# Kernel optimization log

Hardware: AMD Instinct MI355X
Metric: run time of the kernel (lower is better)

## Reference

```python
import jax, jax.numpy as jnp
import numpy as np

N_HEADS, D_MODEL, D_HEAD = 12, 768, 64
INIT_RANGE = 0.02
IGNORE = -100000.0

def setup_inputs() -> dict:
    key = jax.random.key(0)
    ks = jax.random.split(key, 5)
    x = jax.random.normal(ks[0], (4, 2048, D_MODEL), dtype=jnp.float32)
    W_Q = jax.random.normal(ks[1], (N_HEADS, D_MODEL, D_HEAD), dtype=jnp.float32) * INIT_RANGE
    W_K = jax.random.normal(ks[2], (N_HEADS, D_MODEL, D_HEAD), dtype=jnp.float32) * INIT_RANGE
    W_V = jax.random.normal(ks[3], (N_HEADS, D_MODEL, D_HEAD), dtype=jnp.float32) * INIT_RANGE
    W_O = jax.random.normal(ks[4], (N_HEADS, D_HEAD, D_MODEL), dtype=jnp.float32) * INIT_RANGE
    b_Q = jnp.zeros((N_HEADS, D_HEAD), dtype=jnp.float32)
    b_K = jnp.zeros((N_HEADS, D_HEAD), dtype=jnp.float32)
    b_V = jnp.zeros((N_HEADS, D_HEAD), dtype=jnp.float32)
    b_O = jnp.zeros((D_MODEL,), dtype=jnp.float32)
    return {"normalized_resid_pre": x, "W_Q": W_Q, "b_Q": b_Q, "W_K": W_K,
            "b_K": b_K, "W_V": W_V, "b_V": b_V, "W_O": W_O, "b_O": b_O}

def reference(normalized_resid_pre, W_Q, b_Q, W_K, b_K, W_V, b_V, W_O, b_O):
    x = normalized_resid_pre  # [b, s, d_model]
    q = jnp.einsum('bsd,hde->bshe', x, W_Q) + b_Q  # [b, s, h, d_head]
    k = jnp.einsum('bsd,hde->bshe', x, W_K) + b_K
    v = jnp.einsum('bsd,hde->bshe', x, W_V) + b_V
    scores = jnp.einsum('bqhe,bkhe->bhqk', q, k) / jnp.sqrt(jnp.float32(D_HEAD))
    S = x.shape[1]
    causal = jnp.triu(jnp.ones((S, S), dtype=bool), k=1)  # True above diagonal
    scores = jnp.where(causal, jnp.float32(IGNORE), scores)
    pattern = jax.nn.softmax(scores, axis=-1)  # [b, h, q, k]
    z = jnp.einsum('bhqk,bkhe->bqhe', pattern, v)
    attn_out = jnp.einsum('bqhe,hed->bqd', z, W_O) + b_O
    return attn_out
```

## Files before the change

kernel.cpp:

```cpp
#include <hip/hip_runtime.h>

typedef unsigned short u16;
typedef __bf16 bf16x8 __attribute__((ext_vector_type(8)));
typedef float f32x4 __attribute__((ext_vector_type(4)));

#define D_MODEL 768
#define NH 12
#define SEQ 2048
#define BB 4
#define QSCALE 0.18033688011112042f
#define FIXM 8.0f

__device__ __forceinline__ u16 f2b(float f) {
  __bf16 h = (__bf16)f;
  return __builtin_bit_cast(u16, h);
}

__device__ __forceinline__ void gload16(const void* g, void* l) {
  __builtin_amdgcn_global_load_lds((__attribute__((address_space(1))) void*)g,
                                   (__attribute__((address_space(3))) void*)l, 16, 0, 0);
}

__device__ __forceinline__ f32x4 mm16(bf16x8 a, bf16x8 b, f32x4 c) {
  return __builtin_amdgcn_mfma_f32_16x16x32_bf16(a, b, c, 0, 0, 0);
}

__global__ void prep_kernel(const float* __restrict__ x, const float* __restrict__ wq,
                            const float* __restrict__ wk, const float* __restrict__ wv,
                            const float* __restrict__ wo, const float* __restrict__ bq,
                            const float* __restrict__ bk, const float* __restrict__ bv,
                            u16* __restrict__ xb, u16* __restrict__ wt,
                            u16* __restrict__ wot, float* __restrict__ qkvb) {
  const int bid = blockIdx.x;
  if (bid < 6144) {
    int i = (bid * 256 + threadIdx.x) * 4;
    float4 v = *(const float4*)&x[i];
    ushort4 o;
    o.x = f2b(v.x); o.y = f2b(v.y); o.z = f2b(v.z); o.w = f2b(v.w);
    *(ushort4*)&xb[i] = o;
  } else {
    int i = (bid - 6144) * 256 + threadIdx.x;
    {
      int cp = i / 768, d = i % 768;
      int proj = cp / 768, c = cp % 768, h = c / 64, e = c % 64;
      const float* W = (proj == 0) ? wq : ((proj == 1) ? wk : wv);
      float v = W[(size_t)h * 49152 + d * 64 + e];
      if (proj == 0) v *= QSCALE;
      wt[i] = f2b(v);
    }
    if (i < 768 * 768) {
      int rp = i / 768, d = i % 768;
      wot[i] = f2b(wo[(size_t)d * 768 + rp]);
    }
    if (i < 2304) {
      int proj = i / 768, c = i % 768;
      float v = (proj == 0) ? bq[c] * QSCALE : ((proj == 1) ? bk[c] : bv[c]);
      qkvb[i] = v;
    }
  }
}

__global__ __launch_bounds__(512) void gemm_qkv_kernel(
    const u16* __restrict__ A, const u16* __restrict__ Bt,
    const float* __restrict__ qkvb, u16* __restrict__ qw, u16* __restrict__ kw,
    u16* __restrict__ vw) {
  __shared__ u16 lds[73728];
  const int tid = threadIdx.x;
  const int w = tid >> 6, lane = tid & 63;
  const int lg = lane >> 4, cl = lane & 15;
  const int L = blockIdx.x;
  const int v = (L & 7) * 72 + (L >> 3);
  const int bm = v % 9, bn = v / 9;
  const int wr = w >> 1, wc = w & 1;
  const int NT = 12;

  f32x4 vzero = {0.f, 0.f, 0.f, 0.f};
  f32x4 acc[4][4];
#pragma unroll
  for (int mi = 0; mi < 4; mi++)
#pragma unroll
    for (int ni = 0; ni < 4; ni++) acc[mi][ni] = vzero;

  const u16* aB = A + (size_t)bm * 256 * D_MODEL;
  const u16* bB = Bt + (size_t)bn * 128 * D_MODEL;
  const int l8 = lane >> 3, l7 = lane & 7;

  auto stage = [&](int buf, int kt, int half) {
    const int kof = kt * 64;
#pragma unroll
    for (int j2 = 0; j2 < 2; j2++) {
      const int r0 = (w * 4 + half * 2 + j2) * 8;
      gload16(aB + (size_t)(r0 + l8) * D_MODEL + kof + l7 * 8,
              &lds[buf * 16384 + r0 * 64]);
    }
    const int r0b = (w * 2 + half) * 8;
    gload16(bB + (size_t)(r0b + l8) * D_MODEL + kof + l7 * 8,
            &lds[49152 + buf * 8192 + r0b * 64]);
  };

  stage(0, 0, 0); stage(0, 0, 1);
  stage(1, 1, 0); stage(1, 1, 1);
  asm volatile("s_waitcnt vmcnt(6)" ::: "memory");
  __builtin_amdgcn_s_barrier();

  for (int kt = 0; kt < NT; ++kt) {
    const int cA = (kt % 3) * 16384;
    const int cB = 49152 + (kt % 3) * 8192;
    const int nbuf = (kt + 2) % 3;
#pragma unroll
    for (int ks = 0; ks < 2; ks++) {
      bf16x8 af[4], bf4[4];
#pragma unroll
      for (int mi = 0; mi < 4; mi++)
        af[mi] = *(const bf16x8*)&lds[cA + (wr * 64 + mi * 16 + cl) * 64 + ks * 32 + lg * 8];
#pragma unroll
      for (int ni = 0; ni < 4; ni++)
        bf4[ni] = *(const bf16x8*)&lds[cB + (wc * 64 + ni * 16 + cl) * 64 + ks * 32 + lg * 8];
      if (kt + 2 < NT) stage(nbuf, kt + 2, ks);
      if (ks == 1) {
        if (kt + 2 < NT) asm volatile("s_waitcnt vmcnt(6)" ::: "memory");
        else asm volatile("s_waitcnt vmcnt(0)" ::: "memory");
      }
      __builtin_amdgcn_s_barrier();
      __builtin_amdgcn_s_setprio(1);
#pragma unroll
      for (int mi = 0; mi < 4; mi++)
#pragma unroll
        for (int ni = 0; ni < 4; ni++)
          acc[mi][ni] = mm16(af[mi], bf4[ni], acc[mi][ni]);
      __builtin_amdgcn_s_setprio(0);
      __builtin_amdgcn_s_barrier();
    }
  }

  __syncthreads();
  u16* lw = &lds[w * 4096];
  const int cm = bm * 256 + wr * 64;
  const int cn = bn * 128 + wc * 64;
  const int proj = cm / 768;
  const int h = (cm % 768) >> 6;
  const int b = cn >> 11, s_base = cn & 2047;
  const int rlo = lane >> 3, q8 = lane & 7;

  float bz[4][4];
#pragma unroll
  for (int mi = 0; mi < 4; mi++) {
    float4 b4 = *(const float4*)&qkvb[cm + mi * 16 + lg * 4];
    bz[mi][0] = b4.x; bz[mi][1] = b4.y; bz[mi][2] = b4.z; bz[mi][3] = b4.w;
  }

  if (proj < 2) {
#pragma unroll
    for (int mi = 0; mi < 4; mi++) {
      const int e0 = mi * 16 + lg * 4;
#pragma unroll
      for (int ni = 0; ni < 4; ni++) {
        const int s_l = ni * 16 + cl;
        ushort4 pk;
        pk.x = f2b(acc[mi][ni][0] + bz[mi][0]);
        pk.y = f2b(acc[mi][ni][1] + bz[mi][1]);
        pk.z = f2b(acc[mi][ni][2] + bz[mi][2]);
        pk.w = f2b(acc[mi][ni][3] + bz[mi][3]);
        *(ushort4*)&lw[(s_l * 128 + ((e0 * 2) ^ ((s_l & 7) << 4))) >> 1] = pk;
      }
    }
    u16* dst = ((proj == 0) ? qw : kw) + (((size_t)(b * NH + h) * SEQ + s_base) << 6);
#pragma unroll
    for (int it = 0; it < 8; it++) {
      const int row = it * 8 + rlo;
      *(bf16x8*)&dst[row * 64 + q8 * 8] =
          *(const bf16x8*)&lw[(row * 128 + ((q8 * 16) ^ ((row & 7) << 4))) >> 1];
    }
  } else {
#pragma unroll
    for (int mi = 0; mi < 4; mi++)
#pragma unroll
      for (int ni = 0; ni < 4; ni++) {
        const int s_l = ni * 16 + cl;
#pragma unroll
        for (int r = 0; r < 4; r++) {
          const int e_l = mi * 16 + lg * 4 + r;
          lw[(e_l * 128 + ((s_l * 2) ^ ((e_l & 7) << 4))) >> 1] =
              f2b(acc[mi][ni][r] + bz[mi][r]);
        }
      }
    u16* dst = vw + (((size_t)(b * NH + h)) << 17) + s_base;
#pragma unroll
    for (int it = 0; it < 8; it++) {
      const int row = it * 8 + rlo;
      *(bf16x8*)&dst[((size_t)row << 11) + q8 * 8] =
          *(const bf16x8*)&lw[(row * 128 + ((q8 * 16) ^ ((row & 7) << 4))) >> 1];
    }
  }
}

__global__ __launch_bounds__(512) void gemm_out_kernel(
    const u16* __restrict__ A, const u16* __restrict__ Bt,
    const float* __restrict__ bias0, float* __restrict__ outf) {
  __shared__ u16 lds[73728];
  const int tid = threadIdx.x;
  const int w = tid >> 6, lane = tid & 63;
  const int lg = lane >> 4, cl = lane & 15;
  const int L = blockIdx.x;
  const int v = (L & 7) * 24 + (L >> 3);
  const int bm = v / 6, bn = v % 6;
  const int wr = w >> 1, wc = w & 1;
  const int NT = 12;

  f32x4 vzero = {0.f, 0.f, 0.f, 0.f};
  f32x4 acc[4][4];
#pragma unroll
  for (int mi = 0; mi < 4; mi++)
#pragma unroll
    for (int ni = 0; ni < 4; ni++) acc[mi][ni] = vzero;

  const u16* aB = A + (size_t)bm * 256 * D_MODEL;
  const u16* bB = Bt + (size_t)bn * 128 * D_MODEL;
  const int l8 = lane >> 3, l7 = lane & 7;

  auto stage = [&](int buf, int kt, int half) {
    const int kof = kt * 64;
#pragma unroll
    for (int j2 = 0; j2 < 2; j2++) {
      const int r0 = (w * 4 + half * 2 + j2) * 8;
      gload16(aB + (size_t)(r0 + l8) * D_MODEL + kof + l7 * 8,
              &lds[buf * 16384 + r0 * 64]);
    }
    const int r0b = (w * 2 + half) * 8;
    gload16(bB + (size_t)(r0b + l8) * D_MODEL + kof + l7 * 8,
            &lds[49152 + buf * 8192 + r0b * 64]);
  };

  stage(0, 0, 0); stage(0, 0, 1);
  stage(1, 1, 0); stage(1, 1, 1);
  asm volatile("s_waitcnt vmcnt(6)" ::: "memory");
  __builtin_amdgcn_s_barrier();

  for (int kt = 0; kt < NT; ++kt) {
    const int cA = (kt % 3) * 16384;
    const int cB = 49152 + (kt % 3) * 8192;
    const int nbuf = (kt + 2) % 3;
#pragma unroll
    for (int ks = 0; ks < 2; ks++) {
      bf16x8 af[4], bf4[4];
#pragma unroll
      for (int mi = 0; mi < 4; mi++)
        af[mi] = *(const bf16x8*)&lds[cA + (wr * 64 + mi * 16 + cl) * 64 + ks * 32 + lg * 8];
#pragma unroll
      for (int ni = 0; ni < 4; ni++)
        bf4[ni] = *(const bf16x8*)&lds[cB + (wc * 64 + ni * 16 + cl) * 64 + ks * 32 + lg * 8];
      if (kt + 2 < NT) stage(nbuf, kt + 2, ks);
      if (ks == 1) {
        if (kt + 2 < NT) asm volatile("s_waitcnt vmcnt(6)" ::: "memory");
        else asm volatile("s_waitcnt vmcnt(0)" ::: "memory");
      }
      __builtin_amdgcn_s_barrier();
      __builtin_amdgcn_s_setprio(1);
#pragma unroll
      for (int mi = 0; mi < 4; mi++)
#pragma unroll
        for (int ni = 0; ni < 4; ni++)
          acc[mi][ni] = mm16(af[mi], bf4[ni], acc[mi][ni]);
      __builtin_amdgcn_s_setprio(0);
      __builtin_amdgcn_s_barrier();
    }
  }

  __syncthreads();
  u16* lw = &lds[w * 4096];
  float* lwf = (float*)lw;
  const int m_base = bm * 256 + wr * 64;
  const int n0 = bn * 128 + wc * 64;
  const int rlo = lane >> 3, q8 = lane & 7;
#pragma unroll
  for (int hh = 0; hh < 2; hh++) {
#pragma unroll
    for (int nn = 0; nn < 2; nn++) {
      const int ni = hh * 2 + nn;
      const float bz = bias0[n0 + ni * 16 + cl];
      const int col = nn * 16 + cl;
#pragma unroll
      for (int mi = 0; mi < 4; mi++)
#pragma unroll
        for (int r = 0; r < 4; r++) {
          const int row = mi * 16 + lg * 4 + r;
          lwf[(row * 128 + ((col * 4) ^ ((row & 7) << 4))) >> 2] = acc[mi][ni][r] + bz;
        }
    }
#pragma unroll
    for (int it = 0; it < 8; it++) {
      const int row = it * 8 + rlo;
      const int byt = row * 128 + ((q8 * 16) ^ ((row & 7) << 4));
      *(float4*)&outf[(size_t)(m_base + row) * D_MODEL + n0 + hh * 32 + q8 * 4] =
          *(const float4*)((const char*)lwf + byt);
    }
  }
}

__global__ __launch_bounds__(256) void attn_kernel(
    const u16* __restrict__ q_ws, const u16* __restrict__ k_ws,
    const u16* __restrict__ vT_ws, u16* __restrict__ z_ws) {
  __shared__ u16 lk[2][4096];
  __shared__ u16 lv[2][4096];
  __shared__ u16 lp[4096];
  const int tid = threadIdx.x, w = tid >> 6, lane = tid & 63;
  const int lg = lane >> 4, cl = lane & 15, c7 = cl & 7;
  const int L = blockIdx.x;
  const int vv = (L & 7) * 96 + (L >> 3);
  const int pair = vv & 15, bh = vv >> 4;
  const u16* qp = q_ws + (size_t)bh * SEQ * 64;
  const u16* kp = k_ws + (size_t)bh * SEQ * 64;
  const u16* vp = vT_ws + (size_t)bh * 64 * SEQ;
  const int b = bh / NH, h = bh % NH;

  const __bf16 one1 = (__bf16)1.0f;
  const bf16x8 vones = {one1, one1, one1, one1, one1, one1, one1, one1};

  for (int sel = 0; sel < 2; ++sel) {
    const int qt = (sel == 0) ? pair : 31 - pair;
    const int q0 = qt * 64;
    const int qabs = q0 + w * 16 + cl;

    bf16x8 qf[2];
#pragma unroll
    for (int ks = 0; ks < 2; ks++)
      qf[ks] = *(const bf16x8*)&qp[(size_t)(q0 + w * 16 + cl) * 64 + ks * 32 + lg * 8];

    f32x4 vzero = {0.f, 0.f, 0.f, 0.f};
    f32x4 accO[4];
#pragma unroll
    for (int nb = 0; nb < 4; nb++) accO[nb] = vzero;
    f32x4 accS = vzero;

#pragma unroll
    for (int c2 = 0; c2 < 2; c2++) {
      const int ch = w + c2 * 4;
      gload16(kp + (size_t)(lane)*64 + ch * 8, &lk[0][ch * 64 * 8]);
      gload16(vp + (size_t)lane * SEQ + ch * 8, &lv[0][ch * 64 * 8]);
    }
    asm volatile("s_waitcnt vmcnt(0)" ::: "memory");
    __builtin_amdgcn_s_barrier();

    for (int kt = 0; kt <= qt; ++kt) {
      const int cur = kt & 1;
      const int k0 = kt * 64;
      if (kt < qt) {
        const int kn = k0 + 64;
#pragma unroll
        for (int c2 = 0; c2 < 2; c2++) {
          const int ch = w + c2 * 4;
          gload16(kp + (size_t)(kn + lane) * 64 + ch * 8, &lk[cur ^ 1][ch * 64 * 8]);
          gload16(vp + (size_t)lane * SEQ + kn + ch * 8, &lv[cur ^ 1][ch * 64 * 8]);
        }
      }

      f32x4 sa[4];
#pragma unroll
      for (int cb = 0; cb < 4; cb++) sa[cb] = vzero;
      __builtin_amdgcn_s_setprio(1);
#pragma unroll
      for (int ks = 0; ks < 2; ks++) {
#pragma unroll
        for (int cb = 0; cb < 4; cb++) {
          bf16x8 kf = *(const bf16x8*)&lk[cur][((ks * 4 + lg) * 64 + cb * 16 + cl) * 8];
          sa[cb] = mm16(kf, qf[ks], sa[cb]);
        }
      }
      __builtin_amdgcn_s_setprio(0);
      if (kt == qt) {
#pragma unroll
        for (int cb = 0; cb < 4; cb++)
#pragma unroll
          for (int r = 0; r < 4; r++)
            if (k0 + cb * 16 + lg * 4 + r > qabs) sa[cb][r] = -1e30f;
      }

#pragma unroll
      for (int cb = 0; cb < 4; cb++) {
        float p0 = __builtin_amdgcn_exp2f(sa[cb][0] - FIXM);
        float p1 = __builtin_amdgcn_exp2f(sa[cb][1] - FIXM);
        float p2 = __builtin_amdgcn_exp2f(sa[cb][2] - FIXM);
        float p3 = __builtin_amdgcn_exp2f(sa[cb][3] - FIXM);
        ushort4 pk;
        pk.x = f2b(p0); pk.y = f2b(p1); pk.z = f2b(p2); pk.w = f2b(p3);
        *(ushort4*)&lp[w * 1024 + (cl * 128 + ((cb * 32 + lg * 8) ^ (c7 << 4))) / 2] = pk;
      }

      __builtin_amdgcn_s_setprio(1);
#pragma unroll
      for (int ks = 0; ks < 2; ks++) {
        bf16x8 pf = *(const bf16x8*)&lp[w * 1024 +
                                        (cl * 128 + ((ks * 64 + lg * 16) ^ (c7 << 4))) / 2];
#pragma unroll
        for (int nb = 0; nb < 4; nb++) {
          bf16x8 vf = *(const bf16x8*)&lv[cur][((ks * 4 + lg) * 64 + nb * 16 + cl) * 8];
          accO[nb] = mm16(pf, vf, accO[nb]);
        }
        accS = mm16(pf, vones, accS);
      }
      __builtin_amdgcn_s_setprio(0);

      asm volatile("s_waitcnt vmcnt(0)" ::: "memory");
      __builtin_amdgcn_s_barrier();
    }

    float inv[4];
#pragma unroll
    for (int r = 0; r < 4; r++) inv[r] = 1.f / accS[r];
#pragma unroll
    for (int nb = 0; nb < 4; nb++)
#pragma unroll
      for (int r = 0; r < 4; r++) {
        const int qrow = q0 + w * 16 + lg * 4 + r;
        z_ws[((size_t)b * SEQ + qrow) * D_MODEL + h * 64 + nb * 16 + cl] =
            f2b(accO[nb][r] * inv[r]);
      }
  }
}

extern "C" void kernel_launch(void* const* d_in, const int* in_sizes, int n_in,
                              void* d_out, int out_size, void* d_ws, size_t ws_size,
                              hipStream_t stream) {
  const float* x = (const float*)d_in[0];
  const float* wq = (const float*)d_in[1];
  const float* bq = (const float*)d_in[2];
  const float* wk = (const float*)d_in[3];
  const float* bk = (const float*)d_in[4];
  const float* wv = (const float*)d_in[5];
  const float* bv = (const float*)d_in[6];
  const float* wo = (const float*)d_in[7];
  const float* bo = (const float*)d_in[8];
  float* out = (float*)d_out;

  char* ws = (char*)d_ws;
  size_t off = 0;
  auto carve = [&](size_t bytes) -> u16* {
    u16* p = (u16*)(ws + off);
    off += (bytes + 255) & ~(size_t)255;
    return p;
  };
  u16* xb = carve((size_t)8192 * 768 * 2);
  u16* wt = carve((size_t)2304 * 768 * 2);
  u16* wot = carve((size_t)768 * 768 * 2);
  float* qkvb = (float*)carve((size_t)2304 * 4);
  u16* qw = carve((size_t)BB * NH * SEQ * 64 * 2);
  u16* kw = carve((size_t)BB * NH * SEQ * 64 * 2);
  u16* vw = carve((size_t)BB * NH * SEQ * 64 * 2);
  u16* zw = carve((size_t)8192 * 768 * 2);
  if (ws_size < off) return;

  prep_kernel<<<dim3(13056), dim3(256), 0, stream>>>(x, wq, wk, wv, wo, bq, bk, bv,
                                                     xb, wt, wot, qkvb);
  gemm_qkv_kernel<<<dim3(576), dim3(512), 0, stream>>>(wt, xb, qkvb, qw, kw, vw);
  attn_kernel<<<dim3(768), dim3(256), 0, stream>>>(qw, kw, vw, zw);
  gemm_out_kernel<<<dim3(192), dim3(512), 0, stream>>>(zw, wot, bo, out);
}
```

Measured before the change: 151.0 us.

## Give each attention block one query tile and feed P to MFMA from registers

The attention kernel now launches one block per (batch-head, query tile) instead of pairing a short and a long causal tile in one block. The grid doubles, and blocks are ordered longest tile first within each XCD to balance load. When the 16x16x16 bf16 MFMA builtin exists, the exp'd probabilities feed the PV product straight from registers, which removes the LDS round trip through lp and frees that shared memory. The cost is twice as many MFMA instructions with half the K depth, plus a longest-first ordering that relies on the hardware dispatching blocks in order.

```diff
diff --git a/kernel.cpp b/kernel.cpp
--- a/kernel.cpp
+++ b/kernel.cpp
@@ -2,6 +2,7 @@
 
 typedef unsigned short u16;
 typedef __bf16 bf16x8 __attribute__((ext_vector_type(8)));
+typedef short s16x4 __attribute__((ext_vector_type(4)));
 typedef float f32x4 __attribute__((ext_vector_type(4)));
 
 #define D_MODEL 768
@@ -11,6 +12,12 @@
 #define QSCALE 0.18033688011112042f
 #define FIXM 8.0f
 
+#if __has_builtin(__builtin_amdgcn_mfma_f32_16x16x16bf16_1k)
+#define HAVE_MM16 1
+#else
+#define HAVE_MM16 0
+#endif
+
 __device__ __forceinline__ u16 f2b(float f) {
   __bf16 h = (__bf16)f;
   return __builtin_bit_cast(u16, h);
@@ -24,6 +31,12 @@
 __device__ __forceinline__ f32x4 mm16(bf16x8 a, bf16x8 b, f32x4 c) {
   return __builtin_amdgcn_mfma_f32_16x16x32_bf16(a, b, c, 0, 0, 0);
 }
+
+#if HAVE_MM16
+__device__ __forceinline__ f32x4 mm16k(s16x4 a, s16x4 b, f32x4 c) {
+  return __builtin_amdgcn_mfma_f32_16x16x16bf16_1k(a, b, c, 0, 0, 0);
+}
+#endif
 
 __global__ void prep_kernel(const float* __restrict__ x, const float* __restrict__ wq,
                             const float* __restrict__ wk, const float* __restrict__ wv,
@@ -302,120 +315,146 @@
     const u16* __restrict__ vT_ws, u16* __restrict__ z_ws) {
   __shared__ u16 lk[2][4096];
   __shared__ u16 lv[2][4096];
+#if !HAVE_MM16
   __shared__ u16 lp[4096];
+#endif
   const int tid = threadIdx.x, w = tid >> 6, lane = tid & 63;
   const int lg = lane >> 4, cl = lane & 15, c7 = cl & 7;
   const int L = blockIdx.x;
-  const int vv = (L & 7) * 96 + (L >> 3);
-  const int pair = vv & 15, bh = vv >> 4;
+  const int xcd = L & 7, i = L >> 3;
+  const int qt = 31 - (i / 6);
+  const int bh = xcd * 6 + (i % 6);
   const u16* qp = q_ws + (size_t)bh * SEQ * 64;
   const u16* kp = k_ws + (size_t)bh * SEQ * 64;
   const u16* vp = vT_ws + (size_t)bh * 64 * SEQ;
   const int b = bh / NH, h = bh % NH;
 
+  const int q0 = qt * 64;
+  const int qabs = q0 + w * 16 + cl;
+
+  bf16x8 qf[2];
+#pragma unroll
+  for (int ks = 0; ks < 2; ks++)
+    qf[ks] = *(const bf16x8*)&qp[(size_t)(q0 + w * 16 + cl) * 64 + ks * 32 + lg * 8];
+
+  f32x4 vzero = {0.f, 0.f, 0.f, 0.f};
+  f32x4 accO[4];
+#pragma unroll
+  for (int nb = 0; nb < 4; nb++) accO[nb] = vzero;
+  f32x4 accS = vzero;
+
+#if HAVE_MM16
+  const short one_bf = (short)0x3F80;
+  const s16x4 ones4 = {one_bf, one_bf, one_bf, one_bf};
+#else
   const __bf16 one1 = (__bf16)1.0f;
   const bf16x8 vones = {one1, one1, one1, one1, one1, one1, one1, one1};
-
-  for (int sel = 0; sel < 2; ++sel) {
-    const int qt = (sel == 0) ? pair : 31 - pair;
-    const int q0 = qt * 64;
-    const int qabs = q0 + w * 16 + cl;
-
-    bf16x8 qf[2];
-#pragma unroll
-    for (int ks = 0; ks < 2; ks++)
-      qf[ks] = *(const bf16x8*)&qp[(size_t)(q0 + w * 16 + cl) * 64 + ks * 32 + lg * 8];
-
-    f32x4 vzero = {0.f, 0.f, 0.f, 0.f};
-    f32x4 accO[4];
-#pragma unroll
-    for (int nb = 0; nb < 4; nb++) accO[nb] = vzero;
-    f32x4 accS = vzero;
-
-#pragma unroll
-    for (int c2 = 0; c2 < 2; c2++) {
-      const int ch = w + c2 * 4;
-      gload16(kp + (size_t)(lane)*64 + ch * 8, &lk[0][ch * 64 * 8]);
-      gload16(vp + (size_t)lane * SEQ + ch * 8, &lv[0][ch * 64 * 8]);
-    }
+#endif
+
+#pragma unroll
+  for (int c2 = 0; c2 < 2; c2++) {
+    const int ch = w + c2 * 4;
+    gload16(kp + (size_t)(lane)*64 + ch * 8, &lk[0][ch * 64 * 8]);
+    gload16(vp + (size_t)lane * SEQ + ch * 8, &lv[0][ch * 64 * 8]);
+  }
+  asm volatile("s_waitcnt vmcnt(0)" ::: "memory");
+  __builtin_amdgcn_s_barrier();
+
+  for (int kt = 0; kt <= qt; ++kt) {
+    const int cur = kt & 1;
+    const int k0 = kt * 64;
+    if (kt < qt) {
+      const int kn = k0 + 64;
+#pragma unroll
+      for (int c2 = 0; c2 < 2; c2++) {
+        const int ch = w + c2 * 4;
+        gload16(kp + (size_t)(kn + lane) * 64 + ch * 8, &lk[cur ^ 1][ch * 64 * 8]);
+        gload16(vp + (size_t)lane * SEQ + kn + ch * 8, &lv[cur ^ 1][ch * 64 * 8]);
+      }
+    }
+
+    f32x4 sa[4];
+#pragma unroll
+    for (int cb = 0; cb < 4; cb++) sa[cb] = vzero;
+    __builtin_amdgcn_s_setprio(1);
+#pragma unroll
+    for (int ks = 0; ks < 2; ks++) {
+#pragma unroll
+      for (int cb = 0; cb < 4; cb++) {
+        bf16x8 kf = *(const bf16x8*)&lk[cur][((ks * 4 + lg) * 64 + cb * 16 + cl) * 8];
+        sa[cb] = mm16(kf, qf[ks], sa[cb]);
+      }
+    }
+    __builtin_amdgcn_s_setprio(0);
+    if (kt == qt) {
+#pragma unroll
+      for (int cb = 0; cb < 4; cb++)
+#pragma unroll
+        for (int r = 0; r < 4; r++)
+          if (k0 + cb * 16 + lg * 4 + r > qabs) sa[cb][r] = -1e30f;
+    }
+
+#if HAVE_MM16
+    s16x4 pa[4];
+#pragma unroll
+    for (int cb = 0; cb < 4; cb++) {
+#pragma unroll
+      for (int j = 0; j < 4; j++)
+        pa[cb][j] = (short)f2b(__builtin_amdgcn_exp2f(sa[cb][j] - FIXM));
+    }
+    __builtin_amdgcn_s_setprio(1);
+#pragma unroll
+    for (int cb = 0; cb < 4; cb++) {
+      accS = mm16k(pa[cb], ones4, accS);
+#pragma unroll
+      for (int nb = 0; nb < 4; nb++) {
+        const s16x4 vb = *(const s16x4*)&lv[cur][((cb * 2 + (lg >> 1)) * 64 + nb * 16 + cl) * 8 +
+                                                 (lg & 1) * 4];
+        accO[nb] = mm16k(pa[cb], vb, accO[nb]);
+      }
+    }
+    __builtin_amdgcn_s_setprio(0);
+#else
+#pragma unroll
+    for (int cb = 0; cb < 4; cb++) {
+      float p0 = __builtin_amdgcn_exp2f(sa[cb][0] - FIXM);
+      float p1 = __builtin_amdgcn_exp2f(sa[cb][1] - FIXM);
+      float p2 = __builtin_amdgcn_exp2f(sa[cb][2] - FIXM);
+      float p3 = __builtin_amdgcn_exp2f(sa[cb][3] - FIXM);
+      ushort4 pk;
+      pk.x = f2b(p0); pk.y = f2b(p1); pk.z = f2b(p2); pk.w = f2b(p3);
+      *(ushort4*)&lp[w * 1024 + (cl * 128 + ((cb * 32 + lg * 8) ^ (c7 << 4))) / 2] = pk;
+    }
+    __builtin_amdgcn_s_setprio(1);
+#pragma unroll
+    for (int ks = 0; ks < 2; ks++) {
+      bf16x8 pf = *(const bf16x8*)&lp[w * 1024 +
+                                      (cl * 128 + ((ks * 64 + lg * 16) ^ (c7 << 4))) / 2];
+#pragma unroll
+      for (int nb = 0; nb < 4; nb++) {
+        bf16x8 vf = *(const bf16x8*)&lv[cur][((ks * 4 + lg) * 64 + nb * 16 + cl) * 8];
+        accO[nb] = mm16(pf, vf, accO[nb]);
+      }
+      accS = mm16(pf, vones, accS);
+    }
+    __builtin_amdgcn_s_setprio(0);
+#endif
+
     asm volatile("s_waitcnt vmcnt(0)" ::: "memory");
     __builtin_amdgcn_s_barrier();
-
-    for (int kt = 0; kt <= qt; ++kt) {
-      const int cur = kt & 1;
-      const int k0 = kt * 64;
-      if (kt < qt) {
-        const int kn = k0 + 64;
-#pragma unroll
-        for (int c2 = 0; c2 < 2; c2++) {
-          const int ch = w + c2 * 4;
-          gload16(kp + (size_t)(kn + lane) * 64 + ch * 8, &lk[cur ^ 1][ch * 64 * 8]);
-          gload16(vp + (size_t)lane * SEQ + kn + ch * 8, &lv[cur ^ 1][ch * 64 * 8]);
-        }
-      }
-
-      f32x4 sa[4];
-#pragma unroll
-      for (int cb = 0; cb < 4; cb++) sa[cb] = vzero;
-      __builtin_amdgcn_s_setprio(1);
-#pragma unroll
-      for (int ks = 0; ks < 2; ks++) {
-#pragma unroll
-        for (int cb = 0; cb < 4; cb++) {
-          bf16x8 kf = *(const bf16x8*)&lk[cur][((ks * 4 + lg) * 64 + cb * 16 + cl) * 8];
-          sa[cb] = mm16(kf, qf[ks], sa[cb]);
-        }
-      }
-      __builtin_amdgcn_s_setprio(0);
-      if (kt == qt) {
-#pragma unroll
-        for (int cb = 0; cb < 4; cb++)
-#pragma unroll
-          for (int r = 0; r < 4; r++)
-            if (k0 + cb * 16 + lg * 4 + r > qabs) sa[cb][r] = -1e30f;
-      }
-
-#pragma unroll
-      for (int cb = 0; cb < 4; cb++) {
-        float p0 = __builtin_amdgcn_exp2f(sa[cb][0] - FIXM);
-        float p1 = __builtin_amdgcn_exp2f(sa[cb][1] - FIXM);
-        float p2 = __builtin_amdgcn_exp2f(sa[cb][2] - FIXM);
-        float p3 = __builtin_amdgcn_exp2f(sa[cb][3] - FIXM);
-        ushort4 pk;
-        pk.x = f2b(p0); pk.y = f2b(p1); pk.z = f2b(p2); pk.w = f2b(p3);
-        *(ushort4*)&lp[w * 1024 + (cl * 128 + ((cb * 32 + lg * 8) ^ (c7 << 4))) / 2] = pk;
-      }
-
-      __builtin_amdgcn_s_setprio(1);
-#pragma unroll
-      for (int ks = 0; ks < 2; ks++) {
-        bf16x8 pf = *(const bf16x8*)&lp[w * 1024 +
-                                        (cl * 128 + ((ks * 64 + lg * 16) ^ (c7 << 4))) / 2];
-#pragma unroll
-        for (int nb = 0; nb < 4; nb++) {
-          bf16x8 vf = *(const bf16x8*)&lv[cur][((ks * 4 + lg) * 64 + nb * 16 + cl) * 8];
-          accO[nb] = mm16(pf, vf, accO[nb]);
-        }
-        accS = mm16(pf, vones, accS);
-      }
-      __builtin_amdgcn_s_setprio(0);
-
-      asm volatile("s_waitcnt vmcnt(0)" ::: "memory");
-      __builtin_amdgcn_s_barrier();
-    }
-
-    float inv[4];
-#pragma unroll
-    for (int r = 0; r < 4; r++) inv[r] = 1.f / accS[r];
-#pragma unroll
-    for (int nb = 0; nb < 4; nb++)
-#pragma unroll
-      for (int r = 0; r < 4; r++) {
-        const int qrow = q0 + w * 16 + lg * 4 + r;
-        z_ws[((size_t)b * SEQ + qrow) * D_MODEL + h * 64 + nb * 16 + cl] =
-            f2b(accO[nb][r] * inv[r]);
-      }
-  }
+  }
+
+  float inv[4];
+#pragma unroll
+  for (int r = 0; r < 4; r++) inv[r] = 1.f / accS[r];
+#pragma unroll
+  for (int nb = 0; nb < 4; nb++)
+#pragma unroll
+    for (int r = 0; r < 4; r++) {
+      const int qrow = q0 + w * 16 + lg * 4 + r;
+      z_ws[((size_t)b * SEQ + qrow) * D_MODEL + h * 64 + nb * 16 + cl] =
+          f2b(accO[nb][r] * inv[r]);
+    }
 }
 
 extern "C" void kernel_launch(void* const* d_in, const int* in_sizes, int n_in,
@@ -452,6 +491,6 @@
   prep_kernel<<<dim3(13056), dim3(256), 0, stream>>>(x, wq, wk, wv, wo, bq, bk, bv,
                                                      xb, wt, wot, qkvb);
   gemm_qkv_kernel<<<dim3(576), dim3(512), 0, stream>>>(wt, xb, qkvb, qw, kw, vw);
-  attn_kernel<<<dim3(768), dim3(256), 0, stream>>>(qw, kw, vw, zw);
+  attn_kernel<<<dim3(1536), dim3(256), 0, stream>>>(qw, kw, vw, zw);
   gemm_out_kernel<<<dim3(192), dim3(512), 0, stream>>>(zw, wot, bo, out);
 }
```

After: 153.2 us. About the same (+1.5%).
